# Kernel optimization log

Hardware: AMD Instinct MI355X
Metric: run time of the kernel (lower is better)

Reference implementation:

```python
import jax, jax.numpy as jnp
import numpy as np

N, C, L = 4, 256, 4096
RED, NH, CHUNK = 4, 4, 64
HB = min(L // CHUNK + (L // CHUNK) % 2, 128)  # 64 hash buckets
EPS_BN = 1e-5
EPS_NORM = 5e-5
RES_SCALE = 1.0


def _bn(x, g, b, m, v):
    # inference batchnorm over channel dim of [N, C, L]
    scale = g / jnp.sqrt(v + EPS_BN)
    return (x - m[None, :, None]) * scale[None, :, None] + b[None, :, None]


def _conv1d(x, w, pad):
    return jax.lax.conv_general_dilated(x, w, (1,), [(pad, pad)],
                                        dimension_numbers=('NCH', 'OIH', 'NCH'))


def setup_inputs() -> dict:
    key = jax.random.key(0)
    ks = jax.random.split(key, 4)
    Cr = C // RED
    return {
        'x': jax.random.normal(ks[0], (N, C, L), jnp.float32),
        'rot': jax.random.normal(ks[1], (Cr, NH, HB // 2), jnp.float32),
        'w_match': jax.random.normal(ks[2], (Cr, C, 3), jnp.float32) * 0.05,
        'bn1_g': jnp.ones((Cr,), jnp.float32), 'bn1_b': jnp.zeros((Cr,), jnp.float32),
        'bn1_m': jnp.zeros((Cr,), jnp.float32), 'bn1_v': jnp.ones((Cr,), jnp.float32),
        'w_asm': jax.random.normal(ks[3], (C, C, 1), jnp.float32) * 0.05,
        'bn2_g': jnp.ones((C,), jnp.float32), 'bn2_b': jnp.zeros((C,), jnp.float32),
        'bn2_m': jnp.zeros((C,), jnp.float32), 'bn2_v': jnp.ones((C,), jnp.float32),
        'bn3_g': jnp.ones((C,), jnp.float32), 'bn3_b': jnp.zeros((C,), jnp.float32),
        'bn3_m': jnp.zeros((C,), jnp.float32), 'bn3_v': jnp.ones((C,), jnp.float32),
    }


def reference(x, rot, w_match, bn1_g, bn1_b, bn1_m, bn1_v,
              w_asm, bn2_g, bn2_b, bn2_m, bn2_v,
              bn3_g, bn3_b, bn3_m, bn3_v):
    Cr = C // RED
    # conv_match / conv_assembly branches (conv -> BN -> ReLU)
    x_embed = jax.nn.relu(_bn(_conv1d(x, w_match, 1), bn1_g, bn1_b, bn1_m, bn1_v))  # [N,Cr,L]
    y_embed = jax.nn.relu(_bn(_conv1d(x, w_asm, 0), bn2_g, bn2_b, bn2_m, bn2_v))    # [N,C,L]
    x_embed = jnp.transpose(x_embed, (0, 2, 1))  # [N,L,Cr]
    y_embed = jnp.transpose(y_embed, (0, 2, 1))  # [N,L,C]

    # --- LSH hashing: random rotations, cat with negation, argmax bucket ---
    rv = jnp.einsum('ntf,fhi->nhti', x_embed, rot)           # [N,NH,L,HB/2]
    rv = jnp.concatenate([rv, -rv], axis=-1)                  # [N,NH,L,HB]
    codes = jnp.argmax(rv, axis=-1)                           # [N,NH,L]
    codes = codes + jnp.arange(NH, dtype=codes.dtype)[None, :, None]
    codes = codes.reshape(N, NH * L)

    indices = jnp.argsort(codes, axis=-1)
    undo_sort = jnp.argsort(indices, axis=-1)
    mod_idx = indices % L

    xs = jnp.take_along_axis(x_embed, mod_idx[:, :, None], axis=1)  # [N,NH*L,Cr]
    ys = jnp.take_along_axis(y_embed, mod_idx[:, :, None], axis=1)  # [N,NH*L,C]

    nchunks = L // CHUNK  # L divisible by CHUNK -> padding == 0
    xb = xs.reshape(N, NH, nchunks, CHUNK, Cr)
    yb = ys.reshape(N, NH, nchunks, CHUNK, C)

    # F.normalize(p=2, eps=5e-5): x / max(||x||, eps)
    nrm = jnp.linalg.norm(xb, axis=-1, keepdims=True)
    xm = xb / jnp.maximum(nrm, EPS_NORM)

    def adj(t):  # concat current, previous, next bucket along in-chunk axis
        return jnp.concatenate([t, jnp.roll(t, 1, axis=2), jnp.roll(t, -1, axis=2)], axis=3)

    xm = adj(xm)      # [N,NH,K,3*CHUNK,Cr]
    yb3 = adj(yb)     # [N,NH,K,3*CHUNK,C]

    raw = jnp.einsum('bhkie,bhkje->bhkij', xb, xm)            # [N,NH,K,CHUNK,3*CHUNK]
    lse = jax.scipy.special.logsumexp(raw, axis=-1, keepdims=True)
    score = jnp.exp(raw - lse)
    att = jnp.einsum('bhkij,bhkje->bhkie', score, yb3)        # [N,NH,K,CHUNK,C]

    att = att.reshape(N, NH * L, C)
    att = jnp.take_along_axis(att, undo_sort[:, :, None], axis=1).reshape(N, NH, L, C)
    # NOTE: original code does NOT undo-sort bucket_score; replicate faithfully
    bscore = lse.reshape(N, NH, L, 1)
    probs = jax.nn.softmax(bscore, axis=1)
    out = jnp.sum(att * probs, axis=1)                        # [N,L,C]
    out = jnp.transpose(out, (0, 2, 1))                       # [N,C,L]
    out = _bn(out, bn3_g, bn3_b, bn3_m, bn3_v) * RES_SCALE + x
    return out
```

## Files before the change

### kernel.cpp

```cpp
#include <hip/hip_runtime.h>
#include <math.h>

#define NN 4
#define CCH 256
#define LLEN 4096
#define NHEAD 4
#define NHL 16384
#define NBINS 67

__device__ __forceinline__ float4 f4fma(float4 a, float4 b, float4 c) {
  c.x = fmaf(a.x, b.x, c.x);
  c.y = fmaf(a.y, b.y, c.y);
  c.z = fmaf(a.z, b.z, c.z);
  c.w = fmaf(a.w, b.w, c.w);
  return c;
}
__device__ __forceinline__ float4 f4fmas(float s, float4 b, float4 c) {
  c.x = fmaf(s, b.x, c.x);
  c.y = fmaf(s, b.y, c.y);
  c.z = fmaf(s, b.z, c.z);
  c.w = fmaf(s, b.w, c.w);
  return c;
}

__global__ __launch_bounds__(256) void k_conv_match(
    const float* __restrict__ x, const float* __restrict__ w,
    const float* __restrict__ g, const float* __restrict__ b,
    const float* __restrict__ m, const float* __restrict__ v,
    float* __restrict__ xe) {
  __shared__ float xs[256 * 68];
  __shared__ float wl[64 * 193];
  const int tid = threadIdx.x;
  const int n = blockIdx.x >> 6;
  const int l0 = (blockIdx.x & 63) << 6;
  const float* xn = x + (size_t)n * CCH * LLEN;
  for (int idx = tid; idx < 256 * 66; idx += 256) {
    int ci = idx / 66, j = idx - ci * 66;
    int l = l0 + j - 1;
    xs[ci * 68 + j] = (l >= 0 && l < LLEN) ? xn[ci * LLEN + l] : 0.f;
  }
  const int co = tid & 63;
  const int dlg = tid >> 6;
  float acc[16];
#pragma unroll
  for (int q = 0; q < 16; ++q) acc[q] = 0.f;
  for (int cc = 0; cc < 4; ++cc) {
    __syncthreads();
    for (int idx = tid; idx < 12288; idx += 256) {
      int cw = idx / 192, r = idx - cw * 192;
      wl[cw * 193 + r] = w[cw * 768 + cc * 192 + r];
    }
    __syncthreads();
    const float* wbase = &wl[co * 193];
    for (int cil = 0; cil < 64; ++cil) {
      const float* xrow = &xs[(cc * 64 + cil) * 68 + dlg * 16];
      float4 p0 = ((const float4*)xrow)[0];
      float4 p1 = ((const float4*)xrow)[1];
      float4 p2 = ((const float4*)xrow)[2];
      float4 p3 = ((const float4*)xrow)[3];
      float4 p4 = ((const float4*)xrow)[4];
      float xr[20] = {p0.x,p0.y,p0.z,p0.w, p1.x,p1.y,p1.z,p1.w,
                      p2.x,p2.y,p2.z,p2.w, p3.x,p3.y,p3.z,p3.w,
                      p4.x,p4.y,p4.z,p4.w};
      float w0 = wbase[cil*3], w1 = wbase[cil*3+1], w2 = wbase[cil*3+2];
#pragma unroll
      for (int q = 0; q < 16; ++q) {
        acc[q] = fmaf(w0, xr[q], acc[q]);
        acc[q] = fmaf(w1, xr[q+1], acc[q]);
        acc[q] = fmaf(w2, xr[q+2], acc[q]);
      }
    }
  }
  float scale = g[co] * rsqrtf(v[co] + 1e-5f);
  float bias = b[co] - m[co] * scale;
  float* xo = xe + ((size_t)n * LLEN + l0) * 64 + co;
#pragma unroll
  for (int q = 0; q < 16; ++q) {
    float val = acc[q] * scale + bias;
    xo[(dlg * 16 + q) * 64] = val > 0.f ? val : 0.f;
  }
}

__global__ __launch_bounds__(256) void k_conv_asm(
    const float* __restrict__ x, const float* __restrict__ w,
    const float* __restrict__ g, const float* __restrict__ b,
    const float* __restrict__ m, const float* __restrict__ v,
    float* __restrict__ ye) {
  __shared__ float xt[64 * 68];
  __shared__ float wt[2 * 64 * 132];
  const int tid = threadIdx.x;
  const int n = blockIdx.x >> 6;
  const int l0 = (blockIdx.x & 63) << 6;
  const int cg = tid & 31, lt = tid >> 5;
  float4 a0[8], a1[8];
#pragma unroll
  for (int q = 0; q < 8; ++q) { a0[q] = make_float4(0,0,0,0); a1[q] = make_float4(0,0,0,0); }
  for (int cc = 0; cc < 4; ++cc) {
    __syncthreads();
    for (int idx = tid; idx < 4096; idx += 256) {
      int ci = idx >> 6, dl = idx & 63;
      xt[ci * 68 + dl] = x[((size_t)n * 256 + cc * 64 + ci) * 4096 + l0 + dl];
    }
    for (int idx = tid; idx < 16384; idx += 256) {
      int ci = idx & 63, c = idx >> 6;
      int qd = c >> 2;
      int par = qd & 1, qh = qd >> 1, wq = c & 3;
      wt[par * 8448 + ci * 132 + qh * 4 + wq] = w[c * 256 + cc * 64 + ci];
    }
    __syncthreads();
    for (int ci = 0; ci < 64; ++ci) {
      const float4 xv0 = *(const float4*)&xt[ci * 68 + lt * 8];
      const float4 xv1 = *(const float4*)&xt[ci * 68 + lt * 8 + 4];
      const float4 w0 = *(const float4*)&wt[ci * 132 + cg * 4];
      const float4 w1 = *(const float4*)&wt[8448 + ci * 132 + cg * 4];
      float xl[8] = {xv0.x, xv0.y, xv0.z, xv0.w, xv1.x, xv1.y, xv1.z, xv1.w};
#pragma unroll
      for (int q = 0; q < 8; ++q) {
        a0[q] = f4fmas(xl[q], w0, a0[q]);
        a1[q] = f4fmas(xl[q], w1, a1[q]);
      }
    }
  }
  const int c0 = cg * 8;
  float sc[8], bs[8];
#pragma unroll
  for (int u = 0; u < 8; ++u) {
    float s = g[c0+u] * rsqrtf(v[c0+u] + 1e-5f);
    sc[u] = s; bs[u] = b[c0+u] - m[c0+u] * s;
  }
#pragma unroll
  for (int q = 0; q < 8; ++q) {
    int l = l0 + lt * 8 + q;
    float4 o0, o1;
    o0.x = fmaxf(a0[q].x*sc[0]+bs[0], 0.f);
    o0.y = fmaxf(a0[q].y*sc[1]+bs[1], 0.f);
    o0.z = fmaxf(a0[q].z*sc[2]+bs[2], 0.f);
    o0.w = fmaxf(a0[q].w*sc[3]+bs[3], 0.f);
    o1.x = fmaxf(a1[q].x*sc[4]+bs[4], 0.f);
    o1.y = fmaxf(a1[q].y*sc[5]+bs[5], 0.f);
    o1.z = fmaxf(a1[q].z*sc[6]+bs[6], 0.f);
    o1.w = fmaxf(a1[q].w*sc[7]+bs[7], 0.f);
    float4* dst = (float4*)(ye + ((size_t)n * LLEN + l) * 256 + c0);
    dst[0] = o0; dst[1] = o1;
  }
}

__global__ __launch_bounds__(256) void k_codes(
    const float* __restrict__ xe, const float* __restrict__ rot,
    int* __restrict__ codes) {
  __shared__ float xsh[64 * 65];
  const int tid = threadIdx.x;
  const int n = blockIdx.x >> 6;
  const int t0 = (blockIdx.x & 63) << 6;
  for (int idx = tid; idx < 4096; idx += 256) {
    int tt = idx >> 6, f = idx & 63;
    xsh[tt * 65 + f] = xe[((size_t)n * LLEN + t0 + tt) * 64 + f];
  }
  __syncthreads();
  const int tt = tid & 63, h = tid >> 6;
  float rvv[32];
#pragma unroll
  for (int i = 0; i < 32; ++i) rvv[i] = 0.f;
  const float* xr = &xsh[tt * 65];
  for (int f = 0; f < 64; ++f) {
    float xf = xr[f];
    const float* rr = rot + ((f << 2) + h) * 32;
#pragma unroll
    for (int i = 0; i < 32; ++i) rvv[i] = fmaf(xf, rr[i], rvv[i]);
  }
  float best = rvv[0]; int bi = 0;
#pragma unroll
  for (int i = 1; i < 32; ++i) { if (rvv[i] > best) { best = rvv[i]; bi = i; } }
#pragma unroll
  for (int i = 0; i < 32; ++i) { float nv = -rvv[i]; if (nv > best) { best = nv; bi = 32 + i; } }
  codes[n * NHL + h * LLEN + t0 + tt] = bi + h;
}

__global__ __launch_bounds__(256) void k_hist(const int* __restrict__ codes,
                                              int* __restrict__ offs) {
  __shared__ int hist[NBINS];
  const int tid = threadIdx.x;
  const int n = blockIdx.x;
  if (tid < NBINS) hist[tid] = 0;
  __syncthreads();
  const int* cp = codes + n * NHL;
  for (int idx = tid; idx < NHL; idx += 256) atomicAdd(&hist[cp[idx]], 1);
  __syncthreads();
  if (tid == 0) {
    int s = 0;
    for (int c = 0; c < NBINS; ++c) { offs[n * (NBINS + 1) + c] = s; s += hist[c]; }
    offs[n * (NBINS + 1) + NBINS] = s;
  }
}

__global__ __launch_bounds__(64) void k_scatter(const int* __restrict__ codes,
                                                const int* __restrict__ offs,
                                                int* __restrict__ sidx,
                                                int* __restrict__ undo) {
  const int n = blockIdx.x / NBINS;
  const int c = blockIdx.x - n * NBINS;
  const int lane = threadIdx.x;
  const int* cp = codes + n * NHL;
  int base = offs[n * (NBINS + 1) + c];
  for (int ch = 0; ch < NHL / 64; ++ch) {
    int j = (ch << 6) + lane;
    int cv = cp[j];
    unsigned long long mk = __ballot(cv == c);
    if (cv == c) {
      int pos = base + __popcll(mk & ((1ull << lane) - 1ull));
      sidx[n * NHL + pos] = j;
      undo[n * NHL + j] = pos;
    }
    base += __popcll(mk);
  }
}

__global__ __launch_bounds__(256, 2) void k_att2(const float* __restrict__ xe,
                                                 const float* __restrict__ ye,
                                                 const int* __restrict__ sidx,
                                                 float* __restrict__ lseg,
                                                 float* __restrict__ att) {
  __shared__ float score[64 * 193];
  __shared__ float stg[4352];
  __shared__ int   tmap[192];
  __shared__ float rinv_c[64];
  __shared__ float psum[256];
  __shared__ float pm[256], ps[256];
  __shared__ float lse_row[64];
  const int tid = threadIdx.x;
  const int blk = blockIdx.x;
  const int n = blk >> 8, h = (blk >> 6) & 3, k = blk & 63;
  if (tid < 192) {
    int jl = tid & 63;
    int chn = (tid < 64) ? k : ((tid < 128) ? ((k + 63) & 63) : ((k + 1) & 63));
    tmap[tid] = sidx[n * NHL + h * LLEN + chn * 64 + jl] & (LLEN - 1);
  }
  __syncthreads();
  const float* xen = xe + (size_t)n * LLEN * 64;
  const int il = tid & 63, jg = tid >> 6;
  float4 xi[16];
  float ml = -1e30f, sl = 0.f;
  for (int jc = 0; jc < 3; ++jc) {
    if (jc) __syncthreads();
    {
      int r = tid >> 2, c0 = (tid & 3) * 16;
      const float4* src = (const float4*)(xen + (size_t)tmap[jc * 64 + r] * 64 + c0);
      float4* dst = (float4*)&stg[r * 68 + c0];
      dst[0] = src[0]; dst[1] = src[1]; dst[2] = src[2]; dst[3] = src[3];
    }
    __syncthreads();
    {
      int prt = tid >> 6;
      const float4* row = (const float4*)&stg[il * 68 + prt * 16];
      float s = 0.f;
#pragma unroll
      for (int u = 0; u < 4; ++u) {
        float4 vv = row[u];
        s += vv.x*vv.x + vv.y*vv.y + vv.z*vv.z + vv.w*vv.w;
      }
      psum[il * 4 + prt] = s;
    }
    __syncthreads();
    if (tid < 64) {
      float s = psum[tid*4] + psum[tid*4+1] + psum[tid*4+2] + psum[tid*4+3];
      rinv_c[tid] = 1.f / fmaxf(sqrtf(s), 5e-5f);
    }
    if (jc == 0) {
      const float4* xr = (const float4*)&stg[il * 68];
#pragma unroll
      for (int u = 0; u < 16; ++u) xi[u] = xr[u];
    }
    __syncthreads();
    for (int jj = 0; jj < 16; ++jj) {
      int jl2 = jg * 16 + jj;
      const float4* xj = (const float4*)&stg[jl2 * 68];
      float4 d4 = make_float4(0, 0, 0, 0);
#pragma unroll
      for (int u = 0; u < 16; ++u) d4 = f4fma(xi[u], xj[u], d4);
      float d = (d4.x + d4.y + d4.z + d4.w) * rinv_c[jl2];
      score[il * 193 + jc * 64 + jl2] = d;
      if (d > ml) { sl = sl * __expf(ml - d) + 1.f; ml = d; }
      else sl += __expf(d - ml);
    }
  }
  pm[il * 4 + jg] = ml; ps[il * 4 + jg] = sl;
  __syncthreads();
  if (tid < 64) {
    float m0 = pm[tid*4], m1 = pm[tid*4+1], m2 = pm[tid*4+2], m3 = pm[tid*4+3];
    float mm = fmaxf(fmaxf(m0, m1), fmaxf(m2, m3));
    float ss = ps[tid*4]  * __expf(m0 - mm) + ps[tid*4+1] * __expf(m1 - mm)
             + ps[tid*4+2] * __expf(m2 - mm) + ps[tid*4+3] * __expf(m3 - mm);
    float lv = mm + __logf(ss);
    lse_row[tid] = lv;
    lseg[n * NHL + h * LLEN + k * 64 + tid] = lv;
  }
  __syncthreads();
  {
    float lv = lse_row[il];
#pragma unroll
    for (int jc = 0; jc < 3; ++jc)
      for (int jj = 0; jj < 16; ++jj) {
        int o = il * 193 + jc * 64 + jg * 16 + jj;
        score[o] = __expf(score[o] - lv);
      }
  }
  const int it = tid >> 5, cg = tid & 31;
  float4 a0[8], a1[8];
#pragma unroll
  for (int q = 0; q < 8; ++q) { a0[q] = make_float4(0,0,0,0); a1[q] = make_float4(0,0,0,0); }
  const float* yen = ye + (size_t)n * LLEN * 256;
  for (int yt = 0; yt < 12; ++yt) {
    __syncthreads();
    {
      int r = tid >> 4, c0 = (tid & 15) * 16;
      const float4* src = (const float4*)(yen + (size_t)tmap[yt * 16 + r] * 256 + c0);
      float4* dst = (float4*)&stg[r * 260 + c0];
      dst[0] = src[0]; dst[1] = src[1]; dst[2] = src[2]; dst[3] = src[3];
    }
    __syncthreads();
    for (int jj = 0; jj < 16; ++jj) {
      int j = yt * 16 + jj;
      float4 y0 = *(const float4*)&stg[jj * 260 + 4 * cg];
      float4 y1 = *(const float4*)&stg[jj * 260 + 128 + 4 * cg];
#pragma unroll
      for (int q = 0; q < 8; ++q) {
        float s = score[(q * 8 + it) * 193 + j];
        a0[q] = f4fmas(s, y0, a0[q]);
        a1[q] = f4fmas(s, y1, a1[q]);
      }
    }
  }
  float* abase = att + ((size_t)n * NHL + h * LLEN + k * 64) * 256;
#pragma unroll
  for (int q = 0; q < 8; ++q) {
    int i = q * 8 + it;
    *(float4*)(abase + (size_t)i * 256 + 4 * cg) = a0[q];
    *(float4*)(abase + (size_t)i * 256 + 128 + 4 * cg) = a1[q];
  }
}

__global__ __launch_bounds__(256) void k_final2(const float* __restrict__ att,
                                                const int* __restrict__ undo,
                                                const float* __restrict__ lse,
                                                const float* __restrict__ x,
                                                const float* __restrict__ g,
                                                const float* __restrict__ b,
                                                const float* __restrict__ m,
                                                const float* __restrict__ v,
                                                float* __restrict__ out) {
  __shared__ float t[64 * 257];
  __shared__ float wts[64 * 4];
  __shared__ int   pos[64 * 4];
  const int tid = threadIdx.x;
  const int n = blockIdx.x >> 6;
  const int l0 = (blockIdx.x & 63) << 6;
  if (tid < 64) {
    int l = l0 + tid;
    float e0 = lse[n * NHL + l];
    float e1 = lse[n * NHL + LLEN + l];
    float e2 = lse[n * NHL + 2 * LLEN + l];
    float e3 = lse[n * NHL + 3 * LLEN + l];
    float mx = fmaxf(fmaxf(e0, e1), fmaxf(e2, e3));
    float x0 = __expf(e0 - mx), x1 = __expf(e1 - mx), x2 = __expf(e2 - mx), x3 = __expf(e3 - mx);
    float inv = 1.f / (x0 + x1 + x2 + x3);
    wts[tid * 4 + 0] = x0 * inv; wts[tid * 4 + 1] = x1 * inv;
    wts[tid * 4 + 2] = x2 * inv; wts[tid * 4 + 3] = x3 * inv;
    pos[tid * 4 + 0] = undo[n * NHL + l];
    pos[tid * 4 + 1] = undo[n * NHL + LLEN + l];
    pos[tid * 4 + 2] = undo[n * NHL + 2 * LLEN + l];
    pos[tid * 4 + 3] = undo[n * NHL + 3 * LLEN + l];
  }
  __syncthreads();
  {
    const int ll = tid >> 2, part = tid & 3;
    float4 acc[16];
#pragma unroll
    for (int u = 0; u < 16; ++u) acc[u] = make_float4(0, 0, 0, 0);
    const float* an = att + (size_t)n * NHL * 256;
    for (int hh = 0; hh < 4; ++hh) {
      float wv = wts[ll * 4 + hh];
      const float4* row = (const float4*)(an + (size_t)pos[ll * 4 + hh] * 256 + part * 64);
#pragma unroll
      for (int u = 0; u < 16; ++u) acc[u] = f4fmas(wv, row[u], acc[u]);
    }
    float4* dst = (float4*)&t[ll * 257 + part * 64];
#pragma unroll
    for (int u = 0; u < 16; ++u) dst[u] = acc[u];
  }
  __syncthreads();
  for (int idx = tid; idx < 16384; idx += 256) {
    int c = idx >> 6, dl = idx & 63;
    float s = g[c] * rsqrtf(v[c] + 1e-5f);
    float bias = b[c] - m[c] * s;
    size_t o = ((size_t)n * 256 + c) * LLEN + l0 + dl;
    out[o] = t[dl * 257 + c] * s + bias + x[o];
  }
}

extern "C" void kernel_launch(void* const* d_in, const int* in_sizes, int n_in,
                              void* d_out, int out_size, void* d_ws, size_t ws_size,
                              hipStream_t stream) {
  const float* x       = (const float*)d_in[0];
  const float* rot     = (const float*)d_in[1];
  const float* w_match = (const float*)d_in[2];
  const float* bn1_g   = (const float*)d_in[3];
  const float* bn1_b   = (const float*)d_in[4];
  const float* bn1_m   = (const float*)d_in[5];
  const float* bn1_v   = (const float*)d_in[6];
  const float* w_asm   = (const float*)d_in[7];
  const float* bn2_g   = (const float*)d_in[8];
  const float* bn2_b   = (const float*)d_in[9];
  const float* bn2_m   = (const float*)d_in[10];
  const float* bn2_v   = (const float*)d_in[11];
  const float* bn3_g   = (const float*)d_in[12];
  const float* bn3_b   = (const float*)d_in[13];
  const float* bn3_m   = (const float*)d_in[14];
  const float* bn3_v   = (const float*)d_in[15];
  float* out = (float*)d_out;

  float* ws   = (float*)d_ws;
  float* xe   = ws;
  float* ye   = xe + 1048576;
  float* att  = ye + 4194304;
  float* lse  = att + 16777216;
  int* codes  = (int*)(lse + 65536);
  int* sidx   = codes + 65536;
  int* undo   = sidx + 65536;
  int* offs   = undo + 65536;

  k_conv_match<<<256, 256, 0, stream>>>(x, w_match, bn1_g, bn1_b, bn1_m, bn1_v, xe);
  k_conv_asm<<<256, 256, 0, stream>>>(x, w_asm, bn2_g, bn2_b, bn2_m, bn2_v, ye);
  k_codes<<<256, 256, 0, stream>>>(xe, rot, codes);
  k_hist<<<NN, 256, 0, stream>>>(codes, offs);
  k_scatter<<<NN * NBINS, 64, 0, stream>>>(codes, offs, sidx, undo);
  k_att2<<<1024, 256, 0, stream>>>(xe, ye, sidx, lse, att);
  k_final2<<<NN * 64, 256, 0, stream>>>(att, undo, lse, x, bn3_g, bn3_b, bn3_m, bn3_v, out);
}
```

Measured before the change: 491.6 us.

## Use bf16 MFMA for attention-value product and cut LDS in conv kernels

The score-times-value product in the attention kernel now converts probabilities and gathered value rows to bf16 in shared memory and accumulates with 16x16x32 bf16 MFMA instructions instead of scalar fp32 FMAs. The conv_match and conv_asm kernels are restructured to stage smaller input and weight tiles per chunk, shrinking shared memory so more blocks fit per CU. The final gather kernel uses half-size tiles to double the block count. bf16 rounding of scores and values introduces precision loss against the fp32 reference, and conv_asm now takes extra syncs to reload weights in two halves.

```diff
diff --git a/kernel.cpp b/kernel.cpp
--- a/kernel.cpp
+++ b/kernel.cpp
@@ -8,6 +8,9 @@
 #define NHL 16384
 #define NBINS 67
 
+typedef __attribute__((ext_vector_type(8))) short bshort8;
+typedef __attribute__((ext_vector_type(4))) float f32x4;
+
 __device__ __forceinline__ float4 f4fma(float4 a, float4 b, float4 c) {
   c.x = fmaf(a.x, b.x, c.x);
   c.y = fmaf(a.y, b.y, c.y);
@@ -22,23 +25,23 @@
   c.w = fmaf(s, b.w, c.w);
   return c;
 }
-
-__global__ __launch_bounds__(256) void k_conv_match(
+__device__ __forceinline__ unsigned short f2bf(float f) {
+  union { float f; unsigned u; } v; v.f = f;
+  unsigned r = v.u + 0x7FFF + ((v.u >> 16) & 1);
+  return (unsigned short)(r >> 16);
+}
+
+__global__ __launch_bounds__(256, 2) void k_conv_match(
     const float* __restrict__ x, const float* __restrict__ w,
     const float* __restrict__ g, const float* __restrict__ b,
     const float* __restrict__ m, const float* __restrict__ v,
     float* __restrict__ xe) {
-  __shared__ float xs[256 * 68];
+  __shared__ float xs[64 * 68];
   __shared__ float wl[64 * 193];
   const int tid = threadIdx.x;
   const int n = blockIdx.x >> 6;
   const int l0 = (blockIdx.x & 63) << 6;
   const float* xn = x + (size_t)n * CCH * LLEN;
-  for (int idx = tid; idx < 256 * 66; idx += 256) {
-    int ci = idx / 66, j = idx - ci * 66;
-    int l = l0 + j - 1;
-    xs[ci * 68 + j] = (l >= 0 && l < LLEN) ? xn[ci * LLEN + l] : 0.f;
-  }
   const int co = tid & 63;
   const int dlg = tid >> 6;
   float acc[16];
@@ -46,6 +49,11 @@
   for (int q = 0; q < 16; ++q) acc[q] = 0.f;
   for (int cc = 0; cc < 4; ++cc) {
     __syncthreads();
+    for (int idx = tid; idx < 64 * 66; idx += 256) {
+      int ci = idx / 66, j = idx - ci * 66;
+      int l = l0 + j - 1;
+      xs[ci * 68 + j] = (l >= 0 && l < LLEN) ? xn[(cc * 64 + ci) * LLEN + l] : 0.f;
+    }
     for (int idx = tid; idx < 12288; idx += 256) {
       int cw = idx / 192, r = idx - cw * 192;
       wl[cw * 193 + r] = w[cw * 768 + cc * 192 + r];
@@ -53,7 +61,7 @@
     __syncthreads();
     const float* wbase = &wl[co * 193];
     for (int cil = 0; cil < 64; ++cil) {
-      const float* xrow = &xs[(cc * 64 + cil) * 68 + dlg * 16];
+      const float* xrow = &xs[cil * 68 + dlg * 16];
       float4 p0 = ((const float4*)xrow)[0];
       float4 p1 = ((const float4*)xrow)[1];
       float4 p2 = ((const float4*)xrow)[2];
@@ -81,13 +89,13 @@
   }
 }
 
-__global__ __launch_bounds__(256) void k_conv_asm(
+__global__ __launch_bounds__(256, 3) void k_conv_asm(
     const float* __restrict__ x, const float* __restrict__ w,
     const float* __restrict__ g, const float* __restrict__ b,
     const float* __restrict__ m, const float* __restrict__ v,
     float* __restrict__ ye) {
   __shared__ float xt[64 * 68];
-  __shared__ float wt[2 * 64 * 132];
+  __shared__ float wt[64 * 132];
   const int tid = threadIdx.x;
   const int n = blockIdx.x >> 6;
   const int l0 = (blockIdx.x & 63) << 6;
@@ -101,24 +109,34 @@
       int ci = idx >> 6, dl = idx & 63;
       xt[ci * 68 + dl] = x[((size_t)n * 256 + cc * 64 + ci) * 4096 + l0 + dl];
     }
-    for (int idx = tid; idx < 16384; idx += 256) {
-      int ci = idx & 63, c = idx >> 6;
-      int qd = c >> 2;
-      int par = qd & 1, qh = qd >> 1, wq = c & 3;
-      wt[par * 8448 + ci * 132 + qh * 4 + wq] = w[c * 256 + cc * 64 + ci];
+    for (int idx = tid; idx < 8192; idx += 256) {
+      int ci = idx & 63, cl = idx >> 6;
+      int c = ((cl >> 2) << 3) + (cl & 3);
+      wt[ci * 132 + cl] = w[c * 256 + cc * 64 + ci];
     }
     __syncthreads();
     for (int ci = 0; ci < 64; ++ci) {
       const float4 xv0 = *(const float4*)&xt[ci * 68 + lt * 8];
       const float4 xv1 = *(const float4*)&xt[ci * 68 + lt * 8 + 4];
       const float4 w0 = *(const float4*)&wt[ci * 132 + cg * 4];
-      const float4 w1 = *(const float4*)&wt[8448 + ci * 132 + cg * 4];
       float xl[8] = {xv0.x, xv0.y, xv0.z, xv0.w, xv1.x, xv1.y, xv1.z, xv1.w};
 #pragma unroll
-      for (int q = 0; q < 8; ++q) {
-        a0[q] = f4fmas(xl[q], w0, a0[q]);
-        a1[q] = f4fmas(xl[q], w1, a1[q]);
-      }
+      for (int q = 0; q < 8; ++q) a0[q] = f4fmas(xl[q], w0, a0[q]);
+    }
+    __syncthreads();
+    for (int idx = tid; idx < 8192; idx += 256) {
+      int ci = idx & 63, cl = idx >> 6;
+      int c = ((cl >> 2) << 3) + 4 + (cl & 3);
+      wt[ci * 132 + cl] = w[c * 256 + cc * 64 + ci];
+    }
+    __syncthreads();
+    for (int ci = 0; ci < 64; ++ci) {
+      const float4 xv0 = *(const float4*)&xt[ci * 68 + lt * 8];
+      const float4 xv1 = *(const float4*)&xt[ci * 68 + lt * 8 + 4];
+      const float4 w1 = *(const float4*)&wt[ci * 132 + cg * 4];
+      float xl[8] = {xv0.x, xv0.y, xv0.z, xv0.w, xv1.x, xv1.y, xv1.z, xv1.w};
+#pragma unroll
+      for (int q = 0; q < 8; ++q) a1[q] = f4fmas(xl[q], w1, a1[q]);
     }
   }
   const int c0 = cg * 8;
@@ -221,7 +239,7 @@
                                                  float* __restrict__ lseg,
                                                  float* __restrict__ att) {
   __shared__ float score[64 * 193];
-  __shared__ float stg[4352];
+  __shared__ float stg[4608];
   __shared__ int   tmap[192];
   __shared__ float rinv_c[64];
   __shared__ float psum[256];
@@ -295,66 +313,82 @@
     lseg[n * NHL + h * LLEN + k * 64 + tid] = lv;
   }
   __syncthreads();
+  float pbuf[48];
   {
     float lv = lse_row[il];
 #pragma unroll
-    for (int jc = 0; jc < 3; ++jc)
+    for (int jc2 = 0; jc2 < 3; ++jc2)
+#pragma unroll
+      for (int jj = 0; jj < 16; ++jj)
+        pbuf[jc2 * 16 + jj] = __expf(score[il * 193 + jc2 * 64 + jg * 16 + jj] - lv);
+  }
+  __syncthreads();
+  {
+    unsigned short* sb = (unsigned short*)score;
+#pragma unroll
+    for (int jc2 = 0; jc2 < 3; ++jc2)
+#pragma unroll
       for (int jj = 0; jj < 16; ++jj) {
-        int o = il * 193 + jc * 64 + jg * 16 + jj;
-        score[o] = __expf(score[o] - lv);
+        int j = jc2 * 64 + jg * 16 + jj;
+        sb[il * 200 + j] = f2bf(pbuf[jc2 * 16 + jj]);
       }
   }
-  const int it = tid >> 5, cg = tid & 31;
-  float4 a0[8], a1[8];
-#pragma unroll
-  for (int q = 0; q < 8; ++q) { a0[q] = make_float4(0,0,0,0); a1[q] = make_float4(0,0,0,0); }
+  const int wv = tid >> 6, l = tid & 63;
+  f32x4 acc[16];
+#pragma unroll
+  for (int ct = 0; ct < 16; ++ct) acc[ct] = (f32x4){0.f, 0.f, 0.f, 0.f};
+  const unsigned short* sb = (const unsigned short*)score;
+  unsigned short* ysh = (unsigned short*)stg;
   const float* yen = ye + (size_t)n * LLEN * 256;
-  for (int yt = 0; yt < 12; ++yt) {
+  for (int kk = 0; kk < 6; ++kk) {
     __syncthreads();
     {
-      int r = tid >> 4, c0 = (tid & 15) * 16;
-      const float4* src = (const float4*)(yen + (size_t)tmap[yt * 16 + r] * 256 + c0);
-      float4* dst = (float4*)&stg[r * 260 + c0];
-      dst[0] = src[0]; dst[1] = src[1]; dst[2] = src[2]; dst[3] = src[3];
-    }
-    __syncthreads();
-    for (int jj = 0; jj < 16; ++jj) {
-      int j = yt * 16 + jj;
-      float4 y0 = *(const float4*)&stg[jj * 260 + 4 * cg];
-      float4 y1 = *(const float4*)&stg[jj * 260 + 128 + 4 * cg];
-#pragma unroll
-      for (int q = 0; q < 8; ++q) {
-        float s = score[(q * 8 + it) * 193 + j];
-        a0[q] = f4fmas(s, y0, a0[q]);
-        a1[q] = f4fmas(s, y1, a1[q]);
+      int jl = tid & 31, c0 = (tid >> 5) * 32;
+      const float4* src = (const float4*)(yen + (size_t)tmap[kk * 32 + jl] * 256 + c0);
+#pragma unroll
+      for (int u = 0; u < 8; ++u) {
+        float4 yv = src[u];
+        ysh[(c0 + u*4 + 0) * 32 + jl] = f2bf(yv.x);
+        ysh[(c0 + u*4 + 1) * 32 + jl] = f2bf(yv.y);
+        ysh[(c0 + u*4 + 2) * 32 + jl] = f2bf(yv.z);
+        ysh[(c0 + u*4 + 3) * 32 + jl] = f2bf(yv.w);
       }
     }
+    __syncthreads();
+    bshort8 af = *(const bshort8*)&sb[(wv * 16 + (l & 15)) * 200 + kk * 32 + (l >> 4) * 8];
+#pragma unroll
+    for (int ct = 0; ct < 16; ++ct) {
+      bshort8 bf = *(const bshort8*)&ysh[(ct * 16 + (l & 15)) * 32 + (l >> 4) * 8];
+      acc[ct] = __builtin_amdgcn_mfma_f32_16x16x32_bf16(af, bf, acc[ct], 0, 0, 0);
+    }
   }
   float* abase = att + ((size_t)n * NHL + h * LLEN + k * 64) * 256;
 #pragma unroll
-  for (int q = 0; q < 8; ++q) {
-    int i = q * 8 + it;
-    *(float4*)(abase + (size_t)i * 256 + 4 * cg) = a0[q];
-    *(float4*)(abase + (size_t)i * 256 + 128 + 4 * cg) = a1[q];
-  }
-}
-
-__global__ __launch_bounds__(256) void k_final2(const float* __restrict__ att,
-                                                const int* __restrict__ undo,
-                                                const float* __restrict__ lse,
-                                                const float* __restrict__ x,
-                                                const float* __restrict__ g,
-                                                const float* __restrict__ b,
-                                                const float* __restrict__ m,
-                                                const float* __restrict__ v,
-                                                float* __restrict__ out) {
-  __shared__ float t[64 * 257];
-  __shared__ float wts[64 * 4];
-  __shared__ int   pos[64 * 4];
-  const int tid = threadIdx.x;
-  const int n = blockIdx.x >> 6;
-  const int l0 = (blockIdx.x & 63) << 6;
-  if (tid < 64) {
+  for (int ct = 0; ct < 16; ++ct) {
+    int c = ct * 16 + (l & 15);
+    int i0 = wv * 16 + (l >> 4) * 4;
+#pragma unroll
+    for (int r = 0; r < 4; ++r)
+      abase[(size_t)(i0 + r) * 256 + c] = acc[ct][r];
+  }
+}
+
+__global__ __launch_bounds__(256, 2) void k_final3(const float* __restrict__ att,
+                                                   const int* __restrict__ undo,
+                                                   const float* __restrict__ lse,
+                                                   const float* __restrict__ x,
+                                                   const float* __restrict__ g,
+                                                   const float* __restrict__ b,
+                                                   const float* __restrict__ m,
+                                                   const float* __restrict__ v,
+                                                   float* __restrict__ out) {
+  __shared__ float t[32 * 257];
+  __shared__ float wts[32 * 4];
+  __shared__ int   pos[32 * 4];
+  const int tid = threadIdx.x;
+  const int n = blockIdx.x >> 7;
+  const int l0 = (blockIdx.x & 127) << 5;
+  if (tid < 32) {
     int l = l0 + tid;
     float e0 = lse[n * NHL + l];
     float e1 = lse[n * NHL + LLEN + l];
@@ -372,24 +406,24 @@
   }
   __syncthreads();
   {
-    const int ll = tid >> 2, part = tid & 3;
-    float4 acc[16];
-#pragma unroll
-    for (int u = 0; u < 16; ++u) acc[u] = make_float4(0, 0, 0, 0);
+    const int ll = tid & 31, part = tid >> 5;
+    float4 acc[8];
+#pragma unroll
+    for (int u = 0; u < 8; ++u) acc[u] = make_float4(0, 0, 0, 0);
     const float* an = att + (size_t)n * NHL * 256;
     for (int hh = 0; hh < 4; ++hh) {
-      float wv = wts[ll * 4 + hh];
-      const float4* row = (const float4*)(an + (size_t)pos[ll * 4 + hh] * 256 + part * 64);
-#pragma unroll
-      for (int u = 0; u < 16; ++u) acc[u] = f4fmas(wv, row[u], acc[u]);
-    }
-    float4* dst = (float4*)&t[ll * 257 + part * 64];
-#pragma unroll
-    for (int u = 0; u < 16; ++u) dst[u] = acc[u];
-  }
-  __syncthreads();
-  for (int idx = tid; idx < 16384; idx += 256) {
-    int c = idx >> 6, dl = idx & 63;
+      float wvv = wts[ll * 4 + hh];
+      const float4* row = (const float4*)(an + (size_t)pos[ll * 4 + hh] * 256 + part * 32);
+#pragma unroll
+      for (int u = 0; u < 8; ++u) acc[u] = f4fmas(wvv, row[u], acc[u]);
+    }
+    float4* dst = (float4*)&t[ll * 257 + part * 32];
+#pragma unroll
+    for (int u = 0; u < 8; ++u) dst[u] = acc[u];
+  }
+  __syncthreads();
+  for (int idx = tid; idx < 8192; idx += 256) {
+    int c = idx >> 5, dl = idx & 31;
     float s = g[c] * rsqrtf(v[c] + 1e-5f);
     float bias = b[c] - m[c] * s;
     size_t o = ((size_t)n * 256 + c) * LLEN + l0 + dl;
@@ -434,5 +468,5 @@
   k_hist<<<NN, 256, 0, stream>>>(codes, offs);
   k_scatter<<<NN * NBINS, 64, 0, stream>>>(codes, offs, sidx, undo);
   k_att2<<<1024, 256, 0, stream>>>(xe, ye, sidx, lse, att);
-  k_final2<<<NN * 64, 256, 0, stream>>>(att, undo, lse, x, bn3_g, bn3_b, bn3_m, bn3_v, out);
-}
+  k_final3<<<NN * 128, 256, 0, stream>>>(att, undo, lse, x, bn3_g, bn3_b, bn3_m, bn3_v, out);
+}
```

Measured after the change: 421.4 us. 1.17x faster.
